# Performance work log

Measured on AMD Instinct MI355X. Metric: run time of the kernel, lower is better.

## Reference

```python
import jax, jax.numpy as jnp
import numpy as np
import math

L = 4      # model_layers
D = 512    # model_filters
H = 32     # heads = max(D//16, 1)
DH = D // H  # 16
S = 1024   # dataset_dimension == max_len == seq_len
B = 2
EPS = 1e-5


def setup_inputs() -> dict:
    key = jax.random.key(0)
    ks = jax.random.split(key, 12)
    scale = 0.02
    n = lambda k, shape: jax.random.normal(k, shape, dtype=jnp.float32) * scale
    return {
        "x": jax.random.normal(ks[0], (B, S), dtype=jnp.float32),
        "Winit": n(ks[1], (D,)),               # init_linear weight (1->D)
        "binit": jnp.zeros((D,), jnp.float32),
        "Wq": n(ks[2], (L, D, D)), "bq": jnp.zeros((L, D), jnp.float32),
        "Wk": n(ks[3], (L, D, D)), "bk": jnp.zeros((L, D), jnp.float32),
        "Wv": n(ks[4], (L, D, D)), "bv": jnp.zeros((L, D), jnp.float32),
        "Er": jax.random.normal(ks[5], (L, S, DH), dtype=jnp.float32) * scale,
        "Wlin": n(ks[6], (L, D, D)), "blin": jnp.zeros((L, D), jnp.float32),
        "ln_g": jnp.ones((L, D), jnp.float32), "ln_b": jnp.zeros((L, D), jnp.float32),
        "Wout": n(ks[7], (D, 1)),              # output_linear, no bias
    }


def layernorm(x, g, b):
    mu = jnp.mean(x, axis=-1, keepdims=True)
    var = jnp.mean(jnp.square(x - mu), axis=-1, keepdims=True)
    return (x - mu) * jax.lax.rsqrt(var + EPS) * g + b


def rel_attn(h, Wq, bq, Wk, bk, Wv, bv, Er):
    # h: [B, S, D]
    b_, s_, _ = h.shape
    q = (h @ Wq + bq).reshape(b_, s_, H, DH).transpose(0, 2, 1, 3)  # [B,H,S,dh]
    k = (h @ Wk + bk).reshape(b_, s_, H, DH).transpose(0, 2, 1, 3)
    v = (h @ Wv + bv).reshape(b_, s_, H, DH).transpose(0, 2, 1, 3)
    # relative-position term with skew trick (seq_len == max_len -> full Er)
    QEr = jnp.einsum('bhsd,td->bhst', q, Er)                  # [B,H,S,S]
    padded = jnp.pad(QEr, ((0, 0), (0, 0), (0, 0), (1, 0)))   # pad left of last dim
    Srel = padded.reshape(b_, H, s_ + 1, s_)[:, :, 1:, :]     # skew
    scores = (jnp.einsum('bhsd,bhtd->bhst', q, k) + Srel) / math.sqrt(DH)
    mask = jnp.tril(jnp.ones((s_, s_), dtype=bool))           # causal
    scores = jnp.where(mask, scores, -jnp.inf)
    p = jax.nn.softmax(scores, axis=-1)
    o = jnp.einsum('bhst,bhtd->bhsd', p, v)
    return o.transpose(0, 2, 1, 3).reshape(b_, s_, D)


def reference(x, Winit, binit, Wq, bq, Wk, bk, Wv, bv, Er, Wlin, blin, ln_g, ln_b, Wout):
    # init_linear(1->D) on scalar per position, then exact gelu
    h = jax.nn.gelu(x[..., None] * Winit + binit, approximate=False)  # [B,S,D]
    for l in range(L):
        a = rel_attn(h, Wq[l], bq[l], Wk[l], bk[l], Wv[l], bv[l], Er[l])
        y = layernorm(a @ Wlin[l] + blin[l], ln_g[l], ln_b[l])
        h = h + jax.nn.gelu(y, approximate=False)
    return h.sum(axis=-2) @ Wout  # [B,1]
```

## Files before the change

### kernel.cpp

```cpp
#include <hip/hip_runtime.h>
#include <math.h>

#define NL 4
#define DIM 512
#define NH 32
#define DHD 16
#define SEQ 1024
#define NB 2
#define LN_EPS 1e-5f
#define NEGF (-1e30f)
#define QSC 0.36067376022224085f

typedef _Float16 half4 __attribute__((ext_vector_type(4)));
typedef _Float16 half8 __attribute__((ext_vector_type(8)));
typedef float floatx4 __attribute__((ext_vector_type(4)));

__device__ __forceinline__ float gelu_exact(float x) {
    return 0.5f * x * (1.0f + erff(x * 0.70710678118654752f));
}

__global__ __launch_bounds__(256) void k_prep_w(const float* __restrict__ Wq,
        const float* __restrict__ Wk, const float* __restrict__ Wv,
        const float* __restrict__ Wlin, _Float16* __restrict__ Wqkvt,
        _Float16* __restrict__ Wlint) {
    __shared__ _Float16 lt[64][72];
    const int mz = blockIdx.z;
    const int l = mz >> 2, which = mz & 3;
    const float* src = (which == 0) ? Wq : (which == 1) ? Wk : (which == 2) ? Wv : Wlin;
    src += (size_t)l * 262144;
    const float scale = (which == 0) ? QSC : 1.0f;
    _Float16* dst = (which < 3) ? (Wqkvt + (size_t)l * 786432 + (size_t)which * 262144)
                                : (Wlint + (size_t)l * 262144);
    const int k0 = blockIdx.x << 6, n0 = blockIdx.y << 6;
    const int tid = threadIdx.x;
    #pragma unroll
    for (int p = 0; p < 4; p++) {
        int kl = (p << 4) + (tid >> 4);
        int n4 = (tid & 15) << 2;
        float4 wv = *(const float4*)(src + (size_t)(k0 + kl) * 512 + n0 + n4);
        lt[n4 + 0][kl] = (_Float16)(wv.x * scale);
        lt[n4 + 1][kl] = (_Float16)(wv.y * scale);
        lt[n4 + 2][kl] = (_Float16)(wv.z * scale);
        lt[n4 + 3][kl] = (_Float16)(wv.w * scale);
    }
    __syncthreads();
    int nl = tid >> 2, k16 = (tid & 3) << 4;
    float4* d4 = (float4*)(dst + (size_t)(n0 + nl) * 512 + k0 + k16);
    const float4* s4 = (const float4*)&lt[nl][k16];
    d4[0] = s4[0];
    d4[1] = s4[1];
}

__global__ __launch_bounds__(256) void k_prep_small(const float* __restrict__ bq,
        const float* __restrict__ bk, const float* __restrict__ bv,
        const float* __restrict__ Er, float* __restrict__ bqkv,
        _Float16* __restrict__ Erh) {
    int idx = blockIdx.x * 256 + threadIdx.x;
    if (idx < NL * 1536) {
        int l = idx / 1536, j = idx % 1536;
        int which = j >> 9, jj = j & 511;
        float val = (which == 0) ? bq[l * 512 + jj] * QSC
                  : (which == 1) ? bk[l * 512 + jj] : bv[l * 512 + jj];
        bqkv[idx] = val;
    }
    int e = idx - NL * 1536;
    if (e >= 0 && e < NL * SEQ * DHD) Erh[e] = (_Float16)Er[e];
}

__global__ __launch_bounds__(256) void k_init(const float* __restrict__ x,
        const float* __restrict__ Wi, const float* __restrict__ bi,
        float* __restrict__ h, _Float16* __restrict__ hf) {
    int idx = blockIdx.x * 256 + threadIdx.x;
    int d = idx & (DIM - 1);
    int bs = idx >> 9;
    float val = gelu_exact(x[bs] * Wi[d] + bi[d]);
    h[idx] = val;
    hf[idx] = (_Float16)val;
}

template<int F16OUT>
__global__ __launch_bounds__(256) void k_gemm_mfma(const _Float16* __restrict__ A,
        const _Float16* __restrict__ Bt, const float* __restrict__ bias,
        _Float16* __restrict__ o16, float* __restrict__ o32) {
    __shared__ _Float16 As[64][72];
    __shared__ _Float16 Bs[64][72];
    const int tid = threadIdx.x;
    const int w = tid >> 6, lane = tid & 63;
    const int wm = (w & 1) << 5;
    const int wn = (w >> 1) << 5;
    const int nn = lane & 15, qd = lane >> 4;
    const int m0 = blockIdx.x << 6, n0 = blockIdx.y << 6;
    floatx4 acc[2][2] = {};
    for (int k0 = 0; k0 < 512; k0 += 64) {
        __syncthreads();
        #pragma unroll
        for (int r = 0; r < 2; r++) {
            int c = tid + (r << 8);
            int row = c >> 3, k8 = (c & 7) << 3;
            *(half8*)&As[row][k8] = *(const half8*)(A + (size_t)(m0 + row) * 512 + k0 + k8);
            *(half8*)&Bs[row][k8] = *(const half8*)(Bt + (size_t)(n0 + row) * 512 + k0 + k8);
        }
        __syncthreads();
        #pragma unroll
        for (int ks = 0; ks < 2; ks++) {
            half8 af[2], bf[2];
            #pragma unroll
            for (int t = 0; t < 2; t++) {
                af[t] = *(const half8*)&As[wm + (t << 4) + nn][(ks << 5) + (qd << 3)];
                bf[t] = *(const half8*)&Bs[wn + (t << 4) + nn][(ks << 5) + (qd << 3)];
            }
            #pragma unroll
            for (int ti = 0; ti < 2; ti++)
                #pragma unroll
                for (int tj = 0; tj < 2; tj++)
                    acc[ti][tj] = __builtin_amdgcn_mfma_f32_16x16x32_f16(
                            af[ti], bf[tj], acc[ti][tj], 0, 0, 0);
        }
    }
    float bv[2];
    #pragma unroll
    for (int tj = 0; tj < 2; tj++) bv[tj] = bias[n0 + wn + (tj << 4) + nn];
    #pragma unroll
    for (int ti = 0; ti < 2; ti++) {
        int rowg = m0 + wm + (ti << 4) + (qd << 2);
        #pragma unroll
        for (int tj = 0; tj < 2; tj++) {
            int colg = n0 + wn + (tj << 4) + nn;
            #pragma unroll
            for (int r = 0; r < 4; r++) {
                float val = acc[ti][tj][r] + bv[tj];
                if (F16OUT) {
                    int which = colg >> 9, ci = colg & 511;
                    o16[(size_t)which * 1048576 + (size_t)(rowg + r) * 512 + ci] = (_Float16)val;
                } else {
                    o32[(size_t)(rowg + r) * 512 + colg] = val;
                }
            }
        }
    }
}

__global__ __launch_bounds__(256, 4) void k_attn_mfma(const _Float16* __restrict__ q,
        const _Float16* __restrict__ k, const _Float16* __restrict__ v,
        const _Float16* __restrict__ Er, float* __restrict__ Osp,
        float* __restrict__ ml) {
    __shared__ _Float16 Ks[256][20];
    __shared__ _Float16 Vts[16][264];
    __shared__ float Rel[4][16][84];
    const int tid = threadIdx.x;
    const int wid = tid >> 6, lane = tid & 63;
    const int nn = lane & 15, a4 = (lane >> 4) << 2;
    const int b_ = blockIdx.x >> 5, h_ = blockIdx.x & 31;
    const int qt = blockIdx.y, sp = blockIdx.z;
    const int nch = qt + 1;
    const int hsp = (nch + 1) >> 1;
    const int c_lo = sp ? hsp : 0, c_hi = sp ? nch : hsp;
    const int r0 = qt << 6;
    const int s0w = r0 + (wid << 4);
    const int t_ = tid >> 2, c4 = (tid & 3) << 2;

    half4 qf = *(const half4*)(q + ((size_t)(b_ * SEQ + s0w + nn)) * DIM + h_ * DHD + a4);
    floatx4 O = {0.f, 0.f, 0.f, 0.f};
    float m = NEGF, lsum = 0.f;

    for (int cg = c_lo; cg < c_hi; cg += 4) {
        const int cge = (cg + 4 < c_hi) ? (cg + 4) : c_hi;
        __syncthreads();
        for (int g = 0; g < cge - cg; g++) {
            int rl = (g << 6) + t_;
            size_t gb = ((size_t)(b_ * SEQ + (cg << 6) + rl)) * DIM + h_ * DHD + c4;
            *(half4*)&Ks[rl][c4] = *(const half4*)(k + gb);
            half4 vv4 = *(const half4*)(v + gb);
            Vts[c4 + 0][rl] = vv4.x;
            Vts[c4 + 1][rl] = vv4.y;
            Vts[c4 + 2][rl] = vv4.z;
            Vts[c4 + 3][rl] = vv4.w;
        }
        __syncthreads();
        for (int c = cg; c < cge; c++) {
            const int ct = c << 6;
            const int ctl = (c - cg) << 6;
            const int jbw = 1008 - s0w + ct;
            #pragma unroll
            for (int jt = 0; jt < 5; jt++) {
                int j = jbw + (jt << 4) + nn;
                j = (j < SEQ - 1) ? j : (SEQ - 1);
                half4 ef = *(const half4*)(Er + (size_t)j * DHD + a4);
                floatx4 racc = {0.f, 0.f, 0.f, 0.f};
                racc = __builtin_amdgcn_mfma_f32_16x16x16f16(ef, qf, racc, 0, 0, 0);
                *(floatx4*)&Rel[wid][nn][(jt << 4) + a4] = racc;
            }
            float st[4][4];
            const bool diag = (ct == r0);
            #pragma unroll
            for (int tt = 0; tt < 4; tt++) {
                half4 kf = *(const half4*)&Ks[ctl + (tt << 4) + nn][a4];
                floatx4 sacc = {0.f, 0.f, 0.f, 0.f};
                sacc = __builtin_amdgcn_mfma_f32_16x16x16f16(kf, qf, sacc, 0, 0, 0);
                #pragma unroll
                for (int r = 0; r < 4; r++) {
                    int tl = (tt << 4) + a4 + r;
                    float sv = sacc[r] + Rel[wid][nn][15 - nn + tl];
                    if (diag && (tl > (wid << 4) + nn)) sv = NEGF;
                    st[tt][r] = sv;
                }
            }
            float cmax = NEGF;
            #pragma unroll
            for (int tt = 0; tt < 4; tt++)
                #pragma unroll
                for (int r = 0; r < 4; r++) cmax = fmaxf(cmax, st[tt][r]);
            cmax = fmaxf(cmax, __shfl_xor(cmax, 16));
            cmax = fmaxf(cmax, __shfl_xor(cmax, 32));
            float mnew = fmaxf(m, cmax);
            float alpha = exp2f(m - mnew);
            m = mnew;
            float csum = 0.f;
            half4 pf[4];
            #pragma unroll
            for (int tt = 0; tt < 4; tt++) {
                float p0e = exp2f(st[tt][0] - mnew);
                float p1e = exp2f(st[tt][1] - mnew);
                float p2e = exp2f(st[tt][2] - mnew);
                float p3e = exp2f(st[tt][3] - mnew);
                csum += (p0e + p1e) + (p2e + p3e);
                half4 ph4 = {(_Float16)p0e, (_Float16)p1e, (_Float16)p2e, (_Float16)p3e};
                pf[tt] = ph4;
            }
            csum += __shfl_xor(csum, 16);
            csum += __shfl_xor(csum, 32);
            lsum = lsum * alpha + csum;
            O[0] *= alpha; O[1] *= alpha; O[2] *= alpha; O[3] *= alpha;
            #pragma unroll
            for (int tt = 0; tt < 4; tt++) {
                half4 vf = *(const half4*)&Vts[nn][ctl + (tt << 4) + a4];
                O = __builtin_amdgcn_mfma_f32_16x16x16f16(vf, pf[tt], O, 0, 0, 0);
            }
        }
    }
    float* op = Osp + (size_t)sp * 1048576
              + ((size_t)(b_ * SEQ + s0w + nn)) * DIM + h_ * DHD + a4;
    *(float4*)op = make_float4(O[0], O[1], O[2], O[3]);
    if (a4 == 0) {
        float2* mlp = (float2*)ml;
        mlp[((size_t)((sp * NB + b_) * NH + h_)) * SEQ + s0w + nn] = make_float2(m, lsum);
    }
}

__global__ __launch_bounds__(256) void k_attn_merge(const float* __restrict__ Osp,
        const float* __restrict__ ml, _Float16* __restrict__ ah) {
    int idx = blockIdx.x * 256 + threadIdx.x;
    int d4g = (idx & 127) << 2;
    int row = idx >> 7;
    int b = row >> 10, s = row & 1023, h = d4g >> 4;
    const float2* mlp = (const float2*)ml;
    float2 ml0 = mlp[((size_t)((0 * NB + b) * NH + h)) * SEQ + s];
    float2 ml1 = mlp[((size_t)((1 * NB + b) * NH + h)) * SEQ + s];
    float ms = fmaxf(ml0.x, ml1.x);
    float w0 = exp2f(ml0.x - ms), w1 = exp2f(ml1.x - ms);
    float li = ml0.y * w0 + ml1.y * w1;
    float inv = 1.0f / li;
    float4 O0 = *(const float4*)(Osp + (size_t)row * 512 + d4g);
    float4 O1 = *(const float4*)(Osp + 1048576 + (size_t)row * 512 + d4g);
    half4 r = { (_Float16)((O0.x * w0 + O1.x * w1) * inv),
                (_Float16)((O0.y * w0 + O1.y * w1) * inv),
                (_Float16)((O0.z * w0 + O1.z * w1) * inv),
                (_Float16)((O0.w * w0 + O1.w * w1) * inv) };
    *(half4*)(ah + (size_t)row * 512 + d4g) = r;
}

__global__ __launch_bounds__(256) void k_ln_gelu_res(const float* __restrict__ y,
        const float* __restrict__ gam, const float* __restrict__ bet,
        float* __restrict__ h, _Float16* __restrict__ hf) {
    __shared__ float red[8];
    int row = blockIdx.x, tid = threadIdx.x;
    const float* yr = y + (size_t)row * DIM;
    float v0 = yr[tid], v1 = yr[tid + 256];
    float sum = v0 + v1, sq = v0 * v0 + v1 * v1;
    #pragma unroll
    for (int off = 32; off > 0; off >>= 1) {
        sum += __shfl_down(sum, off);
        sq  += __shfl_down(sq, off);
    }
    if ((tid & 63) == 0) { red[tid >> 6] = sum; red[4 + (tid >> 6)] = sq; }
    __syncthreads();
    float ts = red[0] + red[1] + red[2] + red[3];
    float tq = red[4] + red[5] + red[6] + red[7];
    float mu = ts * (1.0f / DIM);
    float var = tq * (1.0f / DIM) - mu * mu;
    float rs = rsqrtf(var + LN_EPS);
    float z0 = (v0 - mu) * rs * gam[tid] + bet[tid];
    float z1 = (v1 - mu) * rs * gam[tid + 256] + bet[tid + 256];
    size_t base = (size_t)row * DIM;
    float nh0 = h[base + tid] + gelu_exact(z0);
    float nh1 = h[base + tid + 256] + gelu_exact(z1);
    h[base + tid] = nh0;
    h[base + tid + 256] = nh1;
    hf[base + tid] = (_Float16)nh0;
    hf[base + tid + 256] = (_Float16)nh1;
}

__global__ __launch_bounds__(256) void k_colsum(const float* __restrict__ h,
        float* __restrict__ partial) {
    int bt = blockIdx.x;
    int b_ = bt >> 4, t = bt & 15;
    int tid = threadIdx.x;
    #pragma unroll
    for (int half = 0; half < 2; half++) {
        int d = half * 256 + tid;
        float acc = 0.f;
        for (int i = 0; i < 64; i++)
            acc += h[((size_t)(b_ * SEQ + t * 64 + i)) * DIM + d];
        partial[(size_t)bt * DIM + d] = acc;
    }
}

__global__ __launch_bounds__(256) void k_final(const float* __restrict__ partial,
        const float* __restrict__ Wout, float* __restrict__ out) {
    __shared__ float red[4][2];
    int tid = threadIdx.x;
    float acc0 = 0.f, acc1 = 0.f;
    #pragma unroll
    for (int half = 0; half < 2; half++) {
        int d = half * 256 + tid;
        float w = Wout[d];
        float s0 = 0.f, s1 = 0.f;
        for (int t = 0; t < 16; t++) {
            s0 += partial[t * DIM + d];
            s1 += partial[(16 + t) * DIM + d];
        }
        acc0 += s0 * w;
        acc1 += s1 * w;
    }
    #pragma unroll
    for (int off = 32; off > 0; off >>= 1) {
        acc0 += __shfl_down(acc0, off);
        acc1 += __shfl_down(acc1, off);
    }
    if ((tid & 63) == 0) { red[tid >> 6][0] = acc0; red[tid >> 6][1] = acc1; }
    __syncthreads();
    if (tid == 0) {
        out[0] = red[0][0] + red[1][0] + red[2][0] + red[3][0];
        out[1] = red[0][1] + red[1][1] + red[2][1] + red[3][1];
    }
}

extern "C" void kernel_launch(void* const* d_in, const int* in_sizes, int n_in,
                              void* d_out, int out_size, void* d_ws, size_t ws_size,
                              hipStream_t stream) {
    const float* x    = (const float*)d_in[0];
    const float* Wi   = (const float*)d_in[1];
    const float* bi   = (const float*)d_in[2];
    const float* Wq   = (const float*)d_in[3];
    const float* bq   = (const float*)d_in[4];
    const float* Wk   = (const float*)d_in[5];
    const float* bk   = (const float*)d_in[6];
    const float* Wv   = (const float*)d_in[7];
    const float* bv   = (const float*)d_in[8];
    const float* Er   = (const float*)d_in[9];
    const float* Wlin = (const float*)d_in[10];
    const float* blin = (const float*)d_in[11];
    const float* lng  = (const float*)d_in[12];
    const float* lnb  = (const float*)d_in[13];
    const float* Wout = (const float*)d_in[14];
    float* out = (float*)d_out;

    float* ws = (float*)d_ws;
    const size_t N1 = 1048576;
    float*     h     = ws;
    _Float16*  hf    = (_Float16*)(ws + N1);
    _Float16*  qh    = (_Float16*)(ws + N1 + N1/2);
    float*     y     = ws + 3 * N1;
    _Float16*  ah    = (_Float16*)(ws + 4 * N1);
    _Float16*  Wqkvt = (_Float16*)(ws + 4 * N1 + N1/2);
    _Float16*  Wlint = (_Float16*)(ws + 6 * N1);
    float*     bqkv  = ws + 6 * N1 + N1/2;
    _Float16*  Erh   = (_Float16*)(ws + 6 * N1 + N1/2 + 8192);
    float*     Osp   = ws + 7 * N1;
    float*     ml    = ws + 9 * N1;
    float*     pa    = ws + 9 * N1 + 262144 + 64;

    k_prep_w<<<dim3(8, 8, 16), dim3(256), 0, stream>>>(Wq, Wk, Wv, Wlin, Wqkvt, Wlint);
    k_prep_small<<<dim3(280), dim3(256), 0, stream>>>(bq, bk, bv, Er, bqkv, Erh);
    k_init<<<dim3(4096), dim3(256), 0, stream>>>(x, Wi, bi, h, hf);
    for (int l = 0; l < NL; l++) {
        k_gemm_mfma<1><<<dim3(32, 24), dim3(256), 0, stream>>>(
                hf, Wqkvt + (size_t)l * 786432, bqkv + l * 1536, qh, nullptr);
        k_attn_mfma<<<dim3(NB * NH, 16, 2), dim3(256), 0, stream>>>(
                qh, qh + 1048576, qh + 2097152, Erh + (size_t)l * 16384, Osp, ml);
        k_attn_merge<<<dim3(1024), dim3(256), 0, stream>>>(Osp, ml, ah);
        k_gemm_mfma<0><<<dim3(32, 8), dim3(256), 0, stream>>>(
                ah, Wlint + (size_t)l * 262144, blin + l * 512, nullptr, y);
        k_ln_gelu_res<<<dim3(NB * SEQ), dim3(256), 0, stream>>>(
                y, lng + l * 512, lnb + l * 512, h, hf);
    }
    k_colsum<<<dim3(32), dim3(256), 0, stream>>>(h, pa);
    k_final<<<dim3(1), dim3(256), 0, stream>>>(pa, Wout, out);
}
```

Baseline: 322.3 us.

## Fuse prep kernels, merge attention split into Wlin GEMM, async-LDS QKV GEMM

Combines the three setup kernels into one launch. Folds the attention split-merge (softmax rescale of the two partial outputs) into the A-tile load of the output-projection GEMM, which removes the intermediate fp16 attention buffer and one launch per layer. Rewrites the QKV GEMM with a 64x128 tile, K-step 32 and direct global-to-LDS async loads, halving its block count. The fused GEMM recomputes merge weights per K-step and reads fp32 partials directly, and the async-load tiles have no padding, so LDS bank conflicts are possible.

```diff
diff --git a/kernel.cpp b/kernel.cpp
--- a/kernel.cpp
+++ b/kernel.cpp
@@ -19,123 +19,130 @@
     return 0.5f * x * (1.0f + erff(x * 0.70710678118654752f));
 }
 
-__global__ __launch_bounds__(256) void k_prep_w(const float* __restrict__ Wq,
+__device__ __forceinline__ void async16(const void* g, void* l) {
+    __builtin_amdgcn_global_load_lds(
+        (const __attribute__((address_space(1))) void*)g,
+        (__attribute__((address_space(3))) void*)l, 16, 0, 0);
+}
+
+__global__ __launch_bounds__(256) void k_prep_all(const float* __restrict__ Wq,
         const float* __restrict__ Wk, const float* __restrict__ Wv,
-        const float* __restrict__ Wlin, _Float16* __restrict__ Wqkvt,
-        _Float16* __restrict__ Wlint) {
+        const float* __restrict__ Wlin, const float* __restrict__ bq,
+        const float* __restrict__ bk, const float* __restrict__ bv,
+        const float* __restrict__ Er, const float* __restrict__ x,
+        const float* __restrict__ Wi, const float* __restrict__ bi,
+        _Float16* __restrict__ Wqkvt, _Float16* __restrict__ Wlint,
+        float* __restrict__ bqkv, _Float16* __restrict__ Erh,
+        float* __restrict__ h, _Float16* __restrict__ hf) {
     __shared__ _Float16 lt[64][72];
-    const int mz = blockIdx.z;
-    const int l = mz >> 2, which = mz & 3;
-    const float* src = (which == 0) ? Wq : (which == 1) ? Wk : (which == 2) ? Wv : Wlin;
-    src += (size_t)l * 262144;
-    const float scale = (which == 0) ? QSC : 1.0f;
-    _Float16* dst = (which < 3) ? (Wqkvt + (size_t)l * 786432 + (size_t)which * 262144)
-                                : (Wlint + (size_t)l * 262144);
-    const int k0 = blockIdx.x << 6, n0 = blockIdx.y << 6;
+    const int u = blockIdx.x;
     const int tid = threadIdx.x;
-    #pragma unroll
-    for (int p = 0; p < 4; p++) {
-        int kl = (p << 4) + (tid >> 4);
-        int n4 = (tid & 15) << 2;
-        float4 wv = *(const float4*)(src + (size_t)(k0 + kl) * 512 + n0 + n4);
-        lt[n4 + 0][kl] = (_Float16)(wv.x * scale);
-        lt[n4 + 1][kl] = (_Float16)(wv.y * scale);
-        lt[n4 + 2][kl] = (_Float16)(wv.z * scale);
-        lt[n4 + 3][kl] = (_Float16)(wv.w * scale);
-    }
-    __syncthreads();
-    int nl = tid >> 2, k16 = (tid & 3) << 4;
-    float4* d4 = (float4*)(dst + (size_t)(n0 + nl) * 512 + k0 + k16);
-    const float4* s4 = (const float4*)&lt[nl][k16];
-    d4[0] = s4[0];
-    d4[1] = s4[1];
-}
-
-__global__ __launch_bounds__(256) void k_prep_small(const float* __restrict__ bq,
-        const float* __restrict__ bk, const float* __restrict__ bv,
-        const float* __restrict__ Er, float* __restrict__ bqkv,
-        _Float16* __restrict__ Erh) {
-    int idx = blockIdx.x * 256 + threadIdx.x;
-    if (idx < NL * 1536) {
-        int l = idx / 1536, j = idx % 1536;
-        int which = j >> 9, jj = j & 511;
-        float val = (which == 0) ? bq[l * 512 + jj] * QSC
-                  : (which == 1) ? bk[l * 512 + jj] : bv[l * 512 + jj];
-        bqkv[idx] = val;
-    }
-    int e = idx - NL * 1536;
-    if (e >= 0 && e < NL * SEQ * DHD) Erh[e] = (_Float16)Er[e];
-}
-
-__global__ __launch_bounds__(256) void k_init(const float* __restrict__ x,
-        const float* __restrict__ Wi, const float* __restrict__ bi,
-        float* __restrict__ h, _Float16* __restrict__ hf) {
-    int idx = blockIdx.x * 256 + threadIdx.x;
-    int d = idx & (DIM - 1);
-    int bs = idx >> 9;
-    float val = gelu_exact(x[bs] * Wi[d] + bi[d]);
-    h[idx] = val;
-    hf[idx] = (_Float16)val;
-}
-
-template<int F16OUT>
-__global__ __launch_bounds__(256) void k_gemm_mfma(const _Float16* __restrict__ A,
+    if (u < 1024) {
+        const int kx = u & 7, ny = (u >> 3) & 7, mz = u >> 6;
+        const int l = mz >> 2, which = mz & 3;
+        const float* src = (which == 0) ? Wq : (which == 1) ? Wk : (which == 2) ? Wv : Wlin;
+        src += (size_t)l * 262144;
+        const float scale = (which == 0) ? QSC : 1.0f;
+        _Float16* dst = (which < 3) ? (Wqkvt + (size_t)l * 786432 + (size_t)which * 262144)
+                                    : (Wlint + (size_t)l * 262144);
+        const int k0 = kx << 6, n0 = ny << 6;
+        #pragma unroll
+        for (int p = 0; p < 4; p++) {
+            int kl = (p << 4) + (tid >> 4);
+            int n4 = (tid & 15) << 2;
+            float4 wv = *(const float4*)(src + (size_t)(k0 + kl) * 512 + n0 + n4);
+            lt[n4 + 0][kl] = (_Float16)(wv.x * scale);
+            lt[n4 + 1][kl] = (_Float16)(wv.y * scale);
+            lt[n4 + 2][kl] = (_Float16)(wv.z * scale);
+            lt[n4 + 3][kl] = (_Float16)(wv.w * scale);
+        }
+        __syncthreads();
+        int nl = tid >> 2, k16 = (tid & 3) << 4;
+        float4* d4 = (float4*)(dst + (size_t)(n0 + nl) * 512 + k0 + k16);
+        const float4* s4 = (const float4*)&lt[nl][k16];
+        d4[0] = s4[0];
+        d4[1] = s4[1];
+    } else if (u < 2048) {
+        int idx0 = ((u - 1024) << 10) + (tid << 2);
+        int d = idx0 & 511, bs = idx0 >> 9;
+        float xs = x[bs];
+        float4 wv = *(const float4*)(Wi + d);
+        float4 bv = *(const float4*)(bi + d);
+        float4 r;
+        r.x = gelu_exact(xs * wv.x + bv.x);
+        r.y = gelu_exact(xs * wv.y + bv.y);
+        r.z = gelu_exact(xs * wv.z + bv.z);
+        r.w = gelu_exact(xs * wv.w + bv.w);
+        *(float4*)(h + idx0) = r;
+        half4 rh = {(_Float16)r.x, (_Float16)r.y, (_Float16)r.z, (_Float16)r.w};
+        *(half4*)(hf + idx0) = rh;
+    } else {
+        int idx = ((u - 2048) << 8) + tid;
+        if (idx < NL * 1536) {
+            int l = idx / 1536, j = idx % 1536;
+            int which = j >> 9, jj = j & 511;
+            float val = (which == 0) ? bq[l * 512 + jj] * QSC
+                      : (which == 1) ? bk[l * 512 + jj] : bv[l * 512 + jj];
+            bqkv[idx] = val;
+        }
+        int e = idx - NL * 1536;
+        if (e >= 0 && e < NL * SEQ * DHD) Erh[e] = (_Float16)Er[e];
+    }
+}
+
+__global__ __launch_bounds__(256) void k_gemm_qkv(const _Float16* __restrict__ A,
         const _Float16* __restrict__ Bt, const float* __restrict__ bias,
-        _Float16* __restrict__ o16, float* __restrict__ o32) {
-    __shared__ _Float16 As[64][72];
-    __shared__ _Float16 Bs[64][72];
+        _Float16* __restrict__ o16) {
+    __shared__ _Float16 As[64 * 32];
+    __shared__ _Float16 Bs[128 * 32];
     const int tid = threadIdx.x;
     const int w = tid >> 6, lane = tid & 63;
-    const int wm = (w & 1) << 5;
-    const int wn = (w >> 1) << 5;
     const int nn = lane & 15, qd = lane >> 4;
-    const int m0 = blockIdx.x << 6, n0 = blockIdx.y << 6;
-    floatx4 acc[2][2] = {};
-    for (int k0 = 0; k0 < 512; k0 += 64) {
-        __syncthreads();
-        #pragma unroll
-        for (int r = 0; r < 2; r++) {
-            int c = tid + (r << 8);
-            int row = c >> 3, k8 = (c & 7) << 3;
-            *(half8*)&As[row][k8] = *(const half8*)(A + (size_t)(m0 + row) * 512 + k0 + k8);
-            *(half8*)&Bs[row][k8] = *(const half8*)(Bt + (size_t)(n0 + row) * 512 + k0 + k8);
-        }
-        __syncthreads();
-        #pragma unroll
-        for (int ks = 0; ks < 2; ks++) {
-            half8 af[2], bf[2];
-            #pragma unroll
-            for (int t = 0; t < 2; t++) {
-                af[t] = *(const half8*)&As[wm + (t << 4) + nn][(ks << 5) + (qd << 3)];
-                bf[t] = *(const half8*)&Bs[wn + (t << 4) + nn][(ks << 5) + (qd << 3)];
-            }
-            #pragma unroll
-            for (int ti = 0; ti < 2; ti++)
-                #pragma unroll
-                for (int tj = 0; tj < 2; tj++)
-                    acc[ti][tj] = __builtin_amdgcn_mfma_f32_16x16x32_f16(
-                            af[ti], bf[tj], acc[ti][tj], 0, 0, 0);
-        }
-    }
-    float bv[2];
-    #pragma unroll
-    for (int tj = 0; tj < 2; tj++) bv[tj] = bias[n0 + wn + (tj << 4) + nn];
+    const int wm = (w & 1) << 5, wn = (w >> 1) << 6;
+    const int m0 = blockIdx.x << 6, n0 = blockIdx.y << 7;
+    const int ar = (w << 4) + (lane >> 2);
+    const int ac = (lane & 3) << 3;
+    const _Float16* Ag  = A  + (size_t)(m0 + ar) * 512 + ac;
+    const _Float16* Bg0 = Bt + (size_t)(n0 + (w << 5) + (lane >> 2)) * 512 + ac;
+    const _Float16* Bg1 = Bg0 + 16 * 512;
+    _Float16* Al  = As + ((w << 4) << 5);
+    _Float16* Bl0 = Bs + ((w << 5) << 5);
+    _Float16* Bl1 = Bl0 + (16 << 5);
+    floatx4 acc[2][4] = {};
+    for (int k0 = 0; k0 < 512; k0 += 32) {
+        __syncthreads();
+        async16(Ag + k0, Al);
+        async16(Bg0 + k0, Bl0);
+        async16(Bg1 + k0, Bl1);
+        __syncthreads();
+        half8 af[2], bf[4];
+        #pragma unroll
+        for (int t = 0; t < 2; t++)
+            af[t] = *(const half8*)&As[((wm + (t << 4) + nn) << 5) + (qd << 3)];
+        #pragma unroll
+        for (int t = 0; t < 4; t++)
+            bf[t] = *(const half8*)&Bs[((wn + (t << 4) + nn) << 5) + (qd << 3)];
+        #pragma unroll
+        for (int ti = 0; ti < 2; ti++)
+            #pragma unroll
+            for (int tj = 0; tj < 4; tj++)
+                acc[ti][tj] = __builtin_amdgcn_mfma_f32_16x16x32_f16(
+                        af[ti], bf[tj], acc[ti][tj], 0, 0, 0);
+    }
+    float bv4[4];
+    #pragma unroll
+    for (int tj = 0; tj < 4; tj++) bv4[tj] = bias[n0 + wn + (tj << 4) + nn];
     #pragma unroll
     for (int ti = 0; ti < 2; ti++) {
         int rowg = m0 + wm + (ti << 4) + (qd << 2);
         #pragma unroll
-        for (int tj = 0; tj < 2; tj++) {
+        for (int tj = 0; tj < 4; tj++) {
             int colg = n0 + wn + (tj << 4) + nn;
-            #pragma unroll
-            for (int r = 0; r < 4; r++) {
-                float val = acc[ti][tj][r] + bv[tj];
-                if (F16OUT) {
-                    int which = colg >> 9, ci = colg & 511;
-                    o16[(size_t)which * 1048576 + (size_t)(rowg + r) * 512 + ci] = (_Float16)val;
-                } else {
-                    o32[(size_t)(rowg + r) * 512 + colg] = val;
-                }
-            }
+            int which = colg >> 9, ci = colg & 511;
+            _Float16* op = o16 + (size_t)which * 1048576 + (size_t)rowg * 512 + ci;
+            #pragma unroll
+            for (int r = 0; r < 4; r++)
+                op[(size_t)r * 512] = (_Float16)(acc[ti][tj][r] + bv4[tj]);
         }
     }
 }
@@ -247,26 +254,76 @@
     }
 }
 
-__global__ __launch_bounds__(256) void k_attn_merge(const float* __restrict__ Osp,
-        const float* __restrict__ ml, _Float16* __restrict__ ah) {
-    int idx = blockIdx.x * 256 + threadIdx.x;
-    int d4g = (idx & 127) << 2;
-    int row = idx >> 7;
-    int b = row >> 10, s = row & 1023, h = d4g >> 4;
+__global__ __launch_bounds__(256) void k_gemm_lin(const float* __restrict__ Osp,
+        const float* __restrict__ ml, const _Float16* __restrict__ Bt,
+        const float* __restrict__ bias, float* __restrict__ y) {
+    __shared__ _Float16 As[64][40];
+    __shared__ _Float16 Bs[64 * 32];
+    const int tid = threadIdx.x;
+    const int w = tid >> 6, lane = tid & 63;
+    const int nn = lane & 15, qd = lane >> 4;
+    const int wm = (w & 1) << 5, wn = (w >> 1) << 5;
+    const int m0 = blockIdx.x << 6, n0 = blockIdx.y << 6;
+    const int sr = tid >> 2, sc8 = (tid & 3) << 3;
+    const int rowg = m0 + sr;
+    const int bb = rowg >> 10, ss = rowg & 1023;
     const float2* mlp = (const float2*)ml;
-    float2 ml0 = mlp[((size_t)((0 * NB + b) * NH + h)) * SEQ + s];
-    float2 ml1 = mlp[((size_t)((1 * NB + b) * NH + h)) * SEQ + s];
-    float ms = fmaxf(ml0.x, ml1.x);
-    float w0 = exp2f(ml0.x - ms), w1 = exp2f(ml1.x - ms);
-    float li = ml0.y * w0 + ml1.y * w1;
-    float inv = 1.0f / li;
-    float4 O0 = *(const float4*)(Osp + (size_t)row * 512 + d4g);
-    float4 O1 = *(const float4*)(Osp + 1048576 + (size_t)row * 512 + d4g);
-    half4 r = { (_Float16)((O0.x * w0 + O1.x * w1) * inv),
-                (_Float16)((O0.y * w0 + O1.y * w1) * inv),
-                (_Float16)((O0.z * w0 + O1.z * w1) * inv),
-                (_Float16)((O0.w * w0 + O1.w * w1) * inv) };
-    *(half4*)(ah + (size_t)row * 512 + d4g) = r;
+    const _Float16* Bg = Bt + (size_t)(n0 + (w << 4) + (lane >> 2)) * 512 + ((lane & 3) << 3);
+    _Float16* Bl = Bs + ((w << 4) << 5);
+    floatx4 acc[2][2] = {};
+    for (int k0 = 0; k0 < 512; k0 += 32) {
+        __syncthreads();
+        async16(Bg + k0, Bl);
+        {
+            int col = k0 + sc8;
+            int hh = col >> 4;
+            float2 ml0 = mlp[((size_t)((0 * NB + bb) * NH + hh)) * SEQ + ss];
+            float2 ml1 = mlp[((size_t)((1 * NB + bb) * NH + hh)) * SEQ + ss];
+            float msx = fmaxf(ml0.x, ml1.x);
+            float w0 = exp2f(ml0.x - msx), w1 = exp2f(ml1.x - msx);
+            float inv = 1.0f / (ml0.y * w0 + ml1.y * w1);
+            w0 *= inv; w1 *= inv;
+            const float* p0 = Osp + (size_t)rowg * 512 + col;
+            const float* p1 = p0 + 1048576;
+            float4 a0 = *(const float4*)(p0);
+            float4 a1 = *(const float4*)(p0 + 4);
+            float4 b0 = *(const float4*)(p1);
+            float4 b1 = *(const float4*)(p1 + 4);
+            half8 av = { (_Float16)(a0.x * w0 + b0.x * w1), (_Float16)(a0.y * w0 + b0.y * w1),
+                         (_Float16)(a0.z * w0 + b0.z * w1), (_Float16)(a0.w * w0 + b0.w * w1),
+                         (_Float16)(a1.x * w0 + b1.x * w1), (_Float16)(a1.y * w0 + b1.y * w1),
+                         (_Float16)(a1.z * w0 + b1.z * w1), (_Float16)(a1.w * w0 + b1.w * w1) };
+            *(half8*)&As[sr][sc8] = av;
+        }
+        __syncthreads();
+        half8 af[2], bf[2];
+        #pragma unroll
+        for (int t = 0; t < 2; t++) {
+            af[t] = *(const half8*)&As[wm + (t << 4) + nn][qd << 3];
+            bf[t] = *(const half8*)&Bs[((wn + (t << 4) + nn) << 5) + (qd << 3)];
+        }
+        #pragma unroll
+        for (int ti = 0; ti < 2; ti++)
+            #pragma unroll
+            for (int tj = 0; tj < 2; tj++)
+                acc[ti][tj] = __builtin_amdgcn_mfma_f32_16x16x32_f16(
+                        af[ti], bf[tj], acc[ti][tj], 0, 0, 0);
+    }
+    float bv2[2];
+    #pragma unroll
+    for (int tj = 0; tj < 2; tj++) bv2[tj] = bias[n0 + wn + (tj << 4) + nn];
+    #pragma unroll
+    for (int ti = 0; ti < 2; ti++) {
+        int rg = m0 + wm + (ti << 4) + (qd << 2);
+        #pragma unroll
+        for (int tj = 0; tj < 2; tj++) {
+            int colg = n0 + wn + (tj << 4) + nn;
+            float* op = y + (size_t)rg * 512 + colg;
+            #pragma unroll
+            for (int r = 0; r < 4; r++)
+                op[(size_t)r * 512] = acc[ti][tj][r] + bv2[tj];
+        }
+    }
 }
 
 __global__ __launch_bounds__(256) void k_ln_gelu_res(const float* __restrict__ y,
@@ -371,7 +428,6 @@
     _Float16*  hf    = (_Float16*)(ws + N1);
     _Float16*  qh    = (_Float16*)(ws + N1 + N1/2);
     float*     y     = ws + 3 * N1;
-    _Float16*  ah    = (_Float16*)(ws + 4 * N1);
     _Float16*  Wqkvt = (_Float16*)(ws + 4 * N1 + N1/2);
     _Float16*  Wlint = (_Float16*)(ws + 6 * N1);
     float*     bqkv  = ws + 6 * N1 + N1/2;
@@ -380,17 +436,15 @@
     float*     ml    = ws + 9 * N1;
     float*     pa    = ws + 9 * N1 + 262144 + 64;
 
-    k_prep_w<<<dim3(8, 8, 16), dim3(256), 0, stream>>>(Wq, Wk, Wv, Wlin, Wqkvt, Wlint);
-    k_prep_small<<<dim3(280), dim3(256), 0, stream>>>(bq, bk, bv, Er, bqkv, Erh);
-    k_init<<<dim3(4096), dim3(256), 0, stream>>>(x, Wi, bi, h, hf);
+    k_prep_all<<<dim3(2328), dim3(256), 0, stream>>>(Wq, Wk, Wv, Wlin, bq, bk, bv,
+            Er, x, Wi, bi, Wqkvt, Wlint, bqkv, Erh, h, hf);
     for (int l = 0; l < NL; l++) {
-        k_gemm_mfma<1><<<dim3(32, 24), dim3(256), 0, stream>>>(
-                hf, Wqkvt + (size_t)l * 786432, bqkv + l * 1536, qh, nullptr);
+        k_gemm_qkv<<<dim3(32, 12), dim3(256), 0, stream>>>(
+                hf, Wqkvt + (size_t)l * 786432, bqkv + l * 1536, qh);
         k_attn_mfma<<<dim3(NB * NH, 16, 2), dim3(256), 0, stream>>>(
                 qh, qh + 1048576, qh + 2097152, Erh + (size_t)l * 16384, Osp, ml);
-        k_attn_merge<<<dim3(1024), dim3(256), 0, stream>>>(Osp, ml, ah);
-        k_gemm_mfma<0><<<dim3(32, 8), dim3(256), 0, stream>>>(
-                ah, Wlint + (size_t)l * 262144, blin + l * 512, nullptr, y);
+        k_gemm_lin<<<dim3(32, 8), dim3(256), 0, stream>>>(
+                Osp, ml, Wlint + (size_t)l * 262144, blin + l * 512, y);
         k_ln_gelu_res<<<dim3(NB * SEQ), dim3(256), 0, stream>>>(
                 y, lng + l * 512, lnb + l * 512, h, hf);
     }
```

Result: slower. 336.8 us (+4.5%).
